# Optimization experiments

Measured on AMD Instinct MI355X. Metric: run time of the kernel, lower is better.

The kernel has to match this reference:

```python
import jax, jax.numpy as jnp
import numpy as np

K = 8       # out_caps
H = 64      # nhidden
TAU = 1.0

def _l2norm(x, eps=1e-12):
    n = jnp.linalg.norm(x, axis=-1, keepdims=True)
    return x / jnp.maximum(n, eps)

def setup_inputs() -> dict:
    key = jax.random.key(0)
    k1, k2, k3, k4 = jax.random.split(key, 4)
    B, N, NB, D = 128, 50, 32, K * H
    return {
        "self_vectors": jax.random.normal(k1, (B, N, D), dtype=jnp.float32),
        "neighbor_vectors": jax.random.normal(k2, (B, N, NB, D), dtype=jnp.float32),
        "W1": jax.random.normal(k3, (D, D), dtype=jnp.float32) * 0.04,
        "b1": jax.random.normal(k4, (D,), dtype=jnp.float32) * 0.01,
        "max_iter": 3,
    }

def reference(self_vectors, neighbor_vectors, W1, b1, max_iter):
    B, N, _ = self_vectors.shape
    NB = neighbor_vectors.shape[2]
    # fc1 + ReLU projections (dropout p=0 -> identity)
    self_z = jax.nn.relu(self_vectors @ W1.T + b1)            # [B,N,K*H]
    neigh_z = jax.nn.relu(neighbor_vectors @ W1.T + b1)       # [B,N,NB,K*H]
    s = _l2norm(self_z.reshape(B, N, K, H))                   # [B,N,K,H]
    nz = _l2norm(neigh_z.reshape(B, N, NB, K, H))             # [B,N,NB,K,H]
    u = None
    for it in range(max_iter):
        if u is None:
            p = jnp.zeros((B, N, NB, K), dtype=s.dtype)
        else:
            p = jnp.einsum('bnmkh,bnkh->bnmk', nz, u)
        p = jax.nn.softmax(p / TAU, axis=-1)                   # softmax over K
        u = jnp.einsum('bnmkh,bnmk->bnkh', nz, p) + s          # sum over neighbors
        if it < max_iter - 1:
            u = _l2norm(u)
    return jax.nn.relu(u.reshape(B, N, K * H))
```

## Files before the change

### kernel.cpp

```cpp
#include <hip/hip_runtime.h>
#include <hip/hip_bf16.h>


#define D_DIM 512
#define BM 64
#define BK 32
#define KSTEPS (D_DIM / BK)

typedef __attribute__((ext_vector_type(8))) short short8;
typedef __attribute__((ext_vector_type(4))) short short4v;
typedef __attribute__((ext_vector_type(4))) float f32x4;

static __device__ __forceinline__ short f2bf(float f) {
    __bf16 b = (__bf16)f;
    return __builtin_bit_cast(short, b);
}
static __device__ __forceinline__ float bf2f(short s) {
    unsigned u = ((unsigned)(unsigned short)s) << 16;
    return __builtin_bit_cast(float, u);
}
static __device__ __forceinline__ void gload_lds16(const void* g, void* l) {
    __builtin_amdgcn_global_load_lds(
        (const __attribute__((address_space(1))) void*)g,
        (__attribute__((address_space(3))) void*)l, 16, 0, 0);
}

__global__ __launch_bounds__(256) void wconv(const float* __restrict__ W,
                                             short* __restrict__ Wb) {
    const int i = (blockIdx.x * 256 + threadIdx.x) * 8;
    const float4 v0 = *reinterpret_cast<const float4*>(W + i);
    const float4 v1 = *reinterpret_cast<const float4*>(W + i + 4);
    short8 o;
    o[0] = f2bf(v0.x); o[1] = f2bf(v0.y); o[2] = f2bf(v0.z); o[3] = f2bf(v0.w);
    o[4] = f2bf(v1.x); o[5] = f2bf(v1.y); o[6] = f2bf(v1.z); o[7] = f2bf(v1.w);
    *reinterpret_cast<short8*>(Wb + i) = o;
}

template <bool FUSED>
__global__ __launch_bounds__(256, 2) void gemm_route(
    const float* __restrict__ A,
    const short* __restrict__ Wb,
    const float* __restrict__ bias,
    short* __restrict__ Zs,
    const short* __restrict__ S,
    const int* __restrict__ miter_ptr,
    float* __restrict__ out)
{
    __shared__ __align__(16) char smem[73728];
    short* const lA = (short*)smem;
    short* const lB = (short*)(smem + 8192);

    const int t = threadIdx.x;
    const int lane = t & 63;
    const int wid = t >> 6;
    const size_t row0 = (size_t)blockIdx.x * BM;
    const int wc = wid * 128;

    const int ar = t >> 2;
    const int ap = t & 3;
    const int ag = (ap - (ar >> 1)) & 3;
    const float* const aPtr = A + (row0 + ar) * D_DIM + ag * 8;

    float4 ra0, ra1;
    auto loadAreg = [&](int k0) {
        ra0 = *reinterpret_cast<const float4*>(aPtr + k0);
        ra1 = *reinterpret_cast<const float4*>(aPtr + k0 + 4);
    };
    auto writeA = [&](int buf) {
        short8 c;
        c[0] = f2bf(ra0.x); c[1] = f2bf(ra0.y); c[2] = f2bf(ra0.z); c[3] = f2bf(ra0.w);
        c[4] = f2bf(ra1.x); c[5] = f2bf(ra1.y); c[6] = f2bf(ra1.z); c[7] = f2bf(ra1.w);
        *reinterpret_cast<short8*>(lA + buf * 2048 + ar * 32 + ap * 8) = c;
    };
    auto stageB = [&](int k0, int buf) {
        #pragma unroll
        for (int i = 0; i < 8; ++i) {
            const int c = wid * 8 + i;
            const int r = c * 16 + (lane >> 2);
            const int p = lane & 3;
            const int g = (p - (r >> 1)) & 3;
            gload_lds16(Wb + (size_t)r * D_DIM + k0 + g * 8,
                        lB + buf * 16384 + c * 512);
        }
    };

    f32x4 acc[4][8] = {};

    auto compute = [&](int buf) {
        const int s_ = lane >> 4;
        short8 af[4], bfr[8];
        #pragma unroll
        for (int m = 0; m < 4; ++m) {
            const int r = m * 16 + (lane & 15);
            af[m] = *reinterpret_cast<const short8*>(
                lA + buf * 2048 + r * 32 + ((s_ + (r >> 1)) & 3) * 8);
        }
        #pragma unroll
        for (int n = 0; n < 8; ++n) {
            const int r = wc + n * 16 + (lane & 15);
            bfr[n] = *reinterpret_cast<const short8*>(
                lB + buf * 16384 + r * 32 + ((s_ + (r >> 1)) & 3) * 8);
        }
        #pragma unroll
        for (int m = 0; m < 4; ++m)
            #pragma unroll
            for (int n = 0; n < 8; ++n)
                acc[m][n] = __builtin_amdgcn_mfma_f32_16x16x32_bf16(
                    af[m], bfr[n], acc[m][n], 0, 0, 0);
    };

    loadAreg(0);
    stageB(0, 0);
    writeA(0);
    __syncthreads();
    int cur = 0;
    for (int tk = 0; tk < KSTEPS; ++tk) {
        if (tk < KSTEPS - 1) {
            loadAreg((tk + 1) * BK);
            stageB((tk + 1) * BK, cur ^ 1);
        }
        compute(cur);
        if (tk < KSTEPS - 1) writeA(cur ^ 1);
        __syncthreads();
        cur ^= 1;
    }

    short* const zbuf = (short*)(smem + 8192);
    const int cb = wc + (lane & 15);
    float bcol[8];
    #pragma unroll
    for (int n = 0; n < 8; ++n) bcol[n] = bias[cb + n * 16];

    #pragma unroll
    for (int m = 0; m < 4; ++m) {
        #pragma unroll
        for (int r = 0; r < 4; ++r) {
            float v[8];
            float ssa = 0.0f, ssb = 0.0f;
            #pragma unroll
            for (int n = 0; n < 4; ++n) {
                v[n] = fmaxf(acc[m][n][r] + bcol[n], 0.0f);
                ssa = fmaf(v[n], v[n], ssa);
            }
            #pragma unroll
            for (int n = 4; n < 8; ++n) {
                v[n] = fmaxf(acc[m][n][r] + bcol[n], 0.0f);
                ssb = fmaf(v[n], v[n], ssb);
            }
            ssa += __shfl_xor(ssa, 1); ssb += __shfl_xor(ssb, 1);
            ssa += __shfl_xor(ssa, 2); ssb += __shfl_xor(ssb, 2);
            ssa += __shfl_xor(ssa, 4); ssb += __shfl_xor(ssb, 4);
            ssa += __shfl_xor(ssa, 8); ssb += __shfl_xor(ssb, 8);
            const float inva = 1.0f / fmaxf(sqrtf(ssa), 1e-12f);
            const float invb = 1.0f / fmaxf(sqrtf(ssb), 1e-12f);
            const int orow = m * 16 + (lane >> 4) * 4 + r;
            if (FUSED) {
                #pragma unroll
                for (int n = 0; n < 4; ++n)
                    zbuf[orow * D_DIM + cb + n * 16] = f2bf(v[n] * inva);
                #pragma unroll
                for (int n = 4; n < 8; ++n)
                    zbuf[orow * D_DIM + cb + n * 16] = f2bf(v[n] * invb);
            } else {
                #pragma unroll
                for (int n = 0; n < 4; ++n)
                    Zs[(row0 + orow) * D_DIM + cb + n * 16] = f2bf(v[n] * inva);
                #pragma unroll
                for (int n = 4; n < 8; ++n)
                    Zs[(row0 + orow) * D_DIM + cb + n * 16] = f2bf(v[n] * invb);
            }
        }
    }

    if (!FUSED) return;
    __syncthreads();

    float* const scratch = (float*)smem;
    const int tt = t & 127;
    const int ssid = t >> 7;
    const size_t site = (size_t)blockIdx.x * 2 + ssid;
    float* const u  = scratch + ssid * 512;
    float* const pp = scratch + 1024 + ssid * 256;
    const short* const zr = zbuf + ssid * 32 * D_DIM;

    const int e = tt * 4;
    const int go = tt >> 4;
    const short4v sv = *reinterpret_cast<const short4v*>(S + site * D_DIM + e);
    const float s0 = bf2f(sv[0]), s1 = bf2f(sv[1]), s2 = bf2f(sv[2]), s3 = bf2f(sv[3]);
    const int miter = *miter_ptr;

    float v0, v1, v2, v3;
    {
        float a0 = 0, a1 = 0, a2 = 0, a3 = 0;
        for (int m = 0; m < 32; ++m) {
            const short4v z = *reinterpret_cast<const short4v*>(zr + m * D_DIM + e);
            a0 += bf2f(z[0]); a1 += bf2f(z[1]); a2 += bf2f(z[2]); a3 += bf2f(z[3]);
        }
        v0 = fmaf(a0, 0.125f, s0); v1 = fmaf(a1, 0.125f, s1);
        v2 = fmaf(a2, 0.125f, s2); v3 = fmaf(a3, 0.125f, s3);
    }

    const int dm = tt >> 2;
    const int ka = (tt & 3) * 2;

    for (int it = 1; it < miter; ++it) {
        float ssum = v0 * v0 + v1 * v1 + v2 * v2 + v3 * v3;
        ssum += __shfl_xor(ssum, 1);
        ssum += __shfl_xor(ssum, 2);
        ssum += __shfl_xor(ssum, 4);
        ssum += __shfl_xor(ssum, 8);
        const float inv = 1.0f / fmaxf(sqrtf(ssum), 1e-12f);
        v0 *= inv; v1 *= inv; v2 *= inv; v3 *= inv;
        *reinterpret_cast<float4*>(u + e) = make_float4(v0, v1, v2, v3);
        __syncthreads();

        const short* const za = zr + dm * D_DIM + ka * 64;
        const float* const ua = u + ka * 64;
        float da = 0, db = 0;
        #pragma unroll
        for (int j = 0; j < 8; ++j) {
            const int jj = ((j + (tt & 7)) & 7) * 8;
            const short8 zva = *reinterpret_cast<const short8*>(za + jj);
            const short8 zvb = *reinterpret_cast<const short8*>(za + 64 + jj);
            const f32x4 uA0 = *reinterpret_cast<const f32x4*>(ua + jj);
            const f32x4 uA1 = *reinterpret_cast<const f32x4*>(ua + jj + 4);
            const f32x4 uB0 = *reinterpret_cast<const f32x4*>(ua + 64 + jj);
            const f32x4 uB1 = *reinterpret_cast<const f32x4*>(ua + 64 + jj + 4);
            #pragma unroll
            for (int q = 0; q < 4; ++q) {
                da = fmaf(bf2f(zva[q]), uA0[q], da);
                da = fmaf(bf2f(zva[q + 4]), uA1[q], da);
                db = fmaf(bf2f(zvb[q]), uB0[q], db);
                db = fmaf(bf2f(zvb[q + 4]), uB1[q], db);
            }
        }
        float mx = fmaxf(da, db);
        mx = fmaxf(mx, __shfl_xor(mx, 1));
        mx = fmaxf(mx, __shfl_xor(mx, 2));
        const float ea = __expf(da - mx), eb = __expf(db - mx);
        float sm_ = ea + eb;
        sm_ += __shfl_xor(sm_, 1);
        sm_ += __shfl_xor(sm_, 2);
        const float rs = 1.0f / sm_;
        *reinterpret_cast<float2*>(pp + dm * 8 + ka) = make_float2(ea * rs, eb * rs);
        __syncthreads();

        float a0 = 0, a1 = 0, a2 = 0, a3 = 0;
        for (int m = 0; m < 32; ++m) {
            const short4v z = *reinterpret_cast<const short4v*>(zr + m * D_DIM + e);
            const float pm = pp[m * 8 + go];
            a0 = fmaf(bf2f(z[0]), pm, a0); a1 = fmaf(bf2f(z[1]), pm, a1);
            a2 = fmaf(bf2f(z[2]), pm, a2); a3 = fmaf(bf2f(z[3]), pm, a3);
        }
        v0 = s0 + a0; v1 = s1 + a1; v2 = s2 + a2; v3 = s3 + a3;
    }

    *reinterpret_cast<float4*>(out + site * D_DIM + e) =
        make_float4(fmaxf(v0, 0.0f), fmaxf(v1, 0.0f), fmaxf(v2, 0.0f), fmaxf(v3, 0.0f));
}

extern "C" void kernel_launch(void* const* d_in, const int* in_sizes, int n_in,
                              void* d_out, int out_size, void* d_ws, size_t ws_size,
                              hipStream_t stream) {
    const float* self_v  = (const float*)d_in[0];
    const float* neigh_v = (const float*)d_in[1];
    const float* W1      = (const float*)d_in[2];
    const float* b1      = (const float*)d_in[3];
    const int*   miter   = (const int*)d_in[4];
    float* out = (float*)d_out;

    const int sites = in_sizes[0] / D_DIM;
    const int nrows = in_sizes[1] / D_DIM;

    short* s  = (short*)d_ws;
    short* Wb = s + (size_t)sites * D_DIM;

    wconv<<<dim3(D_DIM * D_DIM / (256 * 8)), dim3(256), 0, stream>>>(W1, Wb);
    gemm_route<false><<<dim3(sites / BM), dim3(256), 0, stream>>>(
        self_v, Wb, b1, s, nullptr, nullptr, nullptr);
    gemm_route<true><<<dim3(nrows / BM), dim3(256), 0, stream>>>(
        neigh_v, Wb, b1, nullptr, s, miter, out);
}
```

Measured before the change: 283.8 us.

## Stage fp32 A tiles via direct global-to-LDS loads with deeper prefetch pipeline

A tiles are now loaded as fp32 straight into LDS with global_load_lds instead of passing through registers, and converted to bf16 at fragment-read time. The main loop keeps two stages in flight using explicit vmcnt waits and raw barriers, and the loop is fully unrolled. The aim is to free VGPRs and overlap global loads with MFMA work. In exchange LDS use grows to 80KB, which may limit occupancy to one block per CU. The conversion work also moves into the compute loop and is repeated by every wave that reads A.

```diff
diff --git a/kernel.cpp b/kernel.cpp
--- a/kernel.cpp
+++ b/kernel.cpp
@@ -5,7 +5,7 @@
 #define D_DIM 512
 #define BM 64
 #define BK 32
-#define KSTEPS (D_DIM / BK)
+#define KSTEPS 16
 
 typedef __attribute__((ext_vector_type(8))) short short8;
 typedef __attribute__((ext_vector_type(4))) short short4v;
@@ -46,9 +46,9 @@
     const int* __restrict__ miter_ptr,
     float* __restrict__ out)
 {
-    __shared__ __align__(16) char smem[73728];
-    short* const lA = (short*)smem;
-    short* const lB = (short*)(smem + 8192);
+    __shared__ __align__(16) char smem[81920];
+    float* const lAf32 = (float*)smem;
+    short* const lB = (short*)(smem + 16384);
 
     const int t = threadIdx.x;
     const int lane = t & 63;
@@ -56,50 +56,55 @@
     const size_t row0 = (size_t)blockIdx.x * BM;
     const int wc = wid * 128;
 
-    const int ar = t >> 2;
-    const int ap = t & 3;
-    const int ag = (ap - (ar >> 1)) & 3;
-    const float* const aPtr = A + (row0 + ar) * D_DIM + ag * 8;
-
-    float4 ra0, ra1;
-    auto loadAreg = [&](int k0) {
-        ra0 = *reinterpret_cast<const float4*>(aPtr + k0);
-        ra1 = *reinterpret_cast<const float4*>(aPtr + k0 + 4);
-    };
-    auto writeA = [&](int buf) {
-        short8 c;
-        c[0] = f2bf(ra0.x); c[1] = f2bf(ra0.y); c[2] = f2bf(ra0.z); c[3] = f2bf(ra0.w);
-        c[4] = f2bf(ra1.x); c[5] = f2bf(ra1.y); c[6] = f2bf(ra1.z); c[7] = f2bf(ra1.w);
-        *reinterpret_cast<short8*>(lA + buf * 2048 + ar * 32 + ap * 8) = c;
-    };
-    auto stageB = [&](int k0, int buf) {
+    const int cb = wc + (lane & 15);
+    float bcol[8];
+    #pragma unroll
+    for (int n = 0; n < 8; ++n) bcol[n] = bias[cb + n * 16];
+    int miter = 0;
+    if (FUSED) miter = *miter_ptr;
+
+    auto stage = [&](int step, int buf) {
+        const int k0 = (step < KSTEPS ? step : 0) * BK;
         #pragma unroll
         for (int i = 0; i < 8; ++i) {
             const int c = wid * 8 + i;
             const int r = c * 16 + (lane >> 2);
-            const int p = lane & 3;
-            const int g = (p - (r >> 1)) & 3;
+            const int g = ((lane & 3) - (r >> 1)) & 3;
             gload_lds16(Wb + (size_t)r * D_DIM + k0 + g * 8,
                         lB + buf * 16384 + c * 512);
         }
+        #pragma unroll
+        for (int i = 0; i < 2; ++i) {
+            const int c = wid * 2 + i;
+            const int r = c * 8 + (lane >> 3);
+            const int g = ((lane & 7) - 2 * (r & 3)) & 7;
+            gload_lds16(A + (row0 + r) * D_DIM + k0 + g * 4,
+                        lAf32 + buf * 2048 + c * 256);
+        }
     };
 
     f32x4 acc[4][8] = {};
-
     auto compute = [&](int buf) {
-        const int s_ = lane >> 4;
+        const int q = lane >> 4;
         short8 af[4], bfr[8];
         #pragma unroll
         for (int m = 0; m < 4; ++m) {
             const int r = m * 16 + (lane & 15);
-            af[m] = *reinterpret_cast<const short8*>(
-                lA + buf * 2048 + r * 32 + ((s_ + (r >> 1)) & 3) * 8);
+            const float* ap = lAf32 + buf * 2048 + r * 32 + ((q + (r & 3)) & 3) * 8;
+            const f32x4 a0 = *reinterpret_cast<const f32x4*>(ap);
+            const f32x4 a1 = *reinterpret_cast<const f32x4*>(ap + 4);
+            short8 f;
+            f[0] = f2bf(a0[0]); f[1] = f2bf(a0[1]);
+            f[2] = f2bf(a0[2]); f[3] = f2bf(a0[3]);
+            f[4] = f2bf(a1[0]); f[5] = f2bf(a1[1]);
+            f[6] = f2bf(a1[2]); f[7] = f2bf(a1[3]);
+            af[m] = f;
         }
         #pragma unroll
         for (int n = 0; n < 8; ++n) {
             const int r = wc + n * 16 + (lane & 15);
             bfr[n] = *reinterpret_cast<const short8*>(
-                lB + buf * 16384 + r * 32 + ((s_ + (r >> 1)) & 3) * 8);
+                lB + buf * 16384 + r * 32 + ((q + (r >> 1)) & 3) * 8);
         }
         #pragma unroll
         for (int m = 0; m < 4; ++m)
@@ -109,28 +114,23 @@
                     af[m], bfr[n], acc[m][n], 0, 0, 0);
     };
 
-    loadAreg(0);
-    stageB(0, 0);
-    writeA(0);
-    __syncthreads();
-    int cur = 0;
+    stage(0, 0);
+    stage(1, 1);
+    asm volatile("s_waitcnt vmcnt(10)" ::: "memory");
+    __builtin_amdgcn_s_barrier();
+    #pragma unroll
     for (int tk = 0; tk < KSTEPS; ++tk) {
-        if (tk < KSTEPS - 1) {
-            loadAreg((tk + 1) * BK);
-            stageB((tk + 1) * BK, cur ^ 1);
-        }
-        compute(cur);
-        if (tk < KSTEPS - 1) writeA(cur ^ 1);
-        __syncthreads();
-        cur ^= 1;
-    }
-
-    short* const zbuf = (short*)(smem + 8192);
-    const int cb = wc + (lane & 15);
-    float bcol[8];
-    #pragma unroll
-    for (int n = 0; n < 8; ++n) bcol[n] = bias[cb + n * 16];
-
+        compute(tk & 1);
+        asm volatile("s_waitcnt lgkmcnt(0)" ::: "memory");
+        __builtin_amdgcn_s_barrier();
+        stage(tk + 2, tk & 1);
+        asm volatile("s_waitcnt vmcnt(10)" ::: "memory");
+        __builtin_amdgcn_s_barrier();
+    }
+    asm volatile("s_waitcnt vmcnt(0)" ::: "memory");
+    __builtin_amdgcn_s_barrier();
+
+    short* const zbuf = (short*)(smem + 16384);
     #pragma unroll
     for (int m = 0; m < 4; ++m) {
         #pragma unroll
@@ -179,15 +179,15 @@
     const int tt = t & 127;
     const int ssid = t >> 7;
     const size_t site = (size_t)blockIdx.x * 2 + ssid;
-    float* const u  = scratch + ssid * 512;
-    float* const pp = scratch + 1024 + ssid * 256;
+    float* const u_ = scratch + ssid * 512;
+    float* const p_ = (float*)(smem + 4096) + ssid * 256;
     const short* const zr = zbuf + ssid * 32 * D_DIM;
 
     const int e = tt * 4;
     const int go = tt >> 4;
     const short4v sv = *reinterpret_cast<const short4v*>(S + site * D_DIM + e);
-    const float s0 = bf2f(sv[0]), s1 = bf2f(sv[1]), s2 = bf2f(sv[2]), s3 = bf2f(sv[3]);
-    const int miter = *miter_ptr;
+    const float s0 = bf2f(sv[0]), s1 = bf2f(sv[1]);
+    const float s2 = bf2f(sv[2]), s3 = bf2f(sv[3]);
 
     float v0, v1, v2, v3;
     {
@@ -211,11 +211,11 @@
         ssum += __shfl_xor(ssum, 8);
         const float inv = 1.0f / fmaxf(sqrtf(ssum), 1e-12f);
         v0 *= inv; v1 *= inv; v2 *= inv; v3 *= inv;
-        *reinterpret_cast<float4*>(u + e) = make_float4(v0, v1, v2, v3);
+        *reinterpret_cast<float4*>(u_ + e) = make_float4(v0, v1, v2, v3);
         __syncthreads();
 
         const short* const za = zr + dm * D_DIM + ka * 64;
-        const float* const ua = u + ka * 64;
+        const float* const ua = u_ + ka * 64;
         float da = 0, db = 0;
         #pragma unroll
         for (int j = 0; j < 8; ++j) {
@@ -227,11 +227,11 @@
             const f32x4 uB0 = *reinterpret_cast<const f32x4*>(ua + 64 + jj);
             const f32x4 uB1 = *reinterpret_cast<const f32x4*>(ua + 64 + jj + 4);
             #pragma unroll
-            for (int q = 0; q < 4; ++q) {
-                da = fmaf(bf2f(zva[q]), uA0[q], da);
-                da = fmaf(bf2f(zva[q + 4]), uA1[q], da);
-                db = fmaf(bf2f(zvb[q]), uB0[q], db);
-                db = fmaf(bf2f(zvb[q + 4]), uB1[q], db);
+            for (int qq = 0; qq < 4; ++qq) {
+                da = fmaf(bf2f(zva[qq]), uA0[qq], da);
+                da = fmaf(bf2f(zva[qq + 4]), uA1[qq], da);
+                db = fmaf(bf2f(zvb[qq]), uB0[qq], db);
+                db = fmaf(bf2f(zvb[qq + 4]), uB1[qq], db);
             }
         }
         float mx = fmaxf(da, db);
@@ -242,13 +242,13 @@
         sm_ += __shfl_xor(sm_, 1);
         sm_ += __shfl_xor(sm_, 2);
         const float rs = 1.0f / sm_;
-        *reinterpret_cast<float2*>(pp + dm * 8 + ka) = make_float2(ea * rs, eb * rs);
+        *reinterpret_cast<float2*>(p_ + dm * 8 + ka) = make_float2(ea * rs, eb * rs);
         __syncthreads();
 
         float a0 = 0, a1 = 0, a2 = 0, a3 = 0;
         for (int m = 0; m < 32; ++m) {
             const short4v z = *reinterpret_cast<const short4v*>(zr + m * D_DIM + e);
-            const float pm = pp[m * 8 + go];
+            const float pm = p_[m * 8 + go];
             a0 = fmaf(bf2f(z[0]), pm, a0); a1 = fmaf(bf2f(z[1]), pm, a1);
             a2 = fmaf(bf2f(z[2]), pm, a2); a3 = fmaf(bf2f(z[3]), pm, a3);
         }
@@ -256,7 +256,8 @@
     }
 
     *reinterpret_cast<float4*>(out + site * D_DIM + e) =
-        make_float4(fmaxf(v0, 0.0f), fmaxf(v1, 0.0f), fmaxf(v2, 0.0f), fmaxf(v3, 0.0f));
+        make_float4(fmaxf(v0, 0.0f), fmaxf(v1, 0.0f),
+                    fmaxf(v2, 0.0f), fmaxf(v3, 0.0f));
 }
 
 extern "C" void kernel_launch(void* const* d_in, const int* in_sizes, int n_in,
```

Result: faster. 250.5 us (median of 2 runs) (-11.7%).
